# Optimization experiments

Hardware: AMD Instinct MI355X
Metric: run time of the kernel (lower is better)

## Reference

```python
import jax, jax.numpy as jnp
import numpy as np

N = 50000   # nodes
C = 128     # num_channels
E = 800000  # edges (before self loops)
P = 8192    # pos/neg pairs
L = 2       # num_layers
NEG_SLOPE = 0.2  # GATv2Conv default negative_slope


def setup_inputs() -> dict:
    key = jax.random.key(0)
    ks = jax.random.split(key, 10)
    x = jax.random.normal(ks[0], (N, C), dtype=jnp.float32)
    edge_index = jax.random.randint(ks[1], (2, E), 0, N)
    true_pairs = jax.random.randint(ks[2], (P, 2), 0, N)
    false_pairs = jax.random.randint(ks[3], (P, 2), 0, N)
    s = 1.0 / np.sqrt(C)
    # GATv2Conv params per layer (heads=1, share_weights=False): lin_l, lin_r, att, bias
    Wl = jax.random.normal(ks[4], (L, C, C), dtype=jnp.float32) * s
    Wr = jax.random.normal(ks[5], (L, C, C), dtype=jnp.float32) * s
    att_w = jax.random.normal(ks[6], (L, C), dtype=jnp.float32) * s
    bias = jnp.zeros((L, C), dtype=jnp.float32)
    # ConcatAndLogisticScorer classifier: Linear(2C,C) -> ReLU -> Linear(C,1) -> Sigmoid
    W1 = jax.random.normal(ks[7], (2 * C, C), dtype=jnp.float32) * (1.0 / np.sqrt(2 * C))
    b1 = jnp.zeros((C,), dtype=jnp.float32)
    W2 = jax.random.normal(ks[8], (C, 1), dtype=jnp.float32) * s
    b2 = jnp.zeros((1,), dtype=jnp.float32)
    return dict(x=x, edge_index=edge_index, true_pairs=true_pairs, false_pairs=false_pairs,
                Wl=Wl, Wr=Wr, att_w=att_w, bias=bias, W1=W1, b1=b1, W2=W2, b2=b2)


def _gatv2_layer(h, src, dst, Wl, Wr, a, b):
    # single-head GATv2: e_ij = a^T LeakyReLU(Wl h_j + Wr h_i); softmax over incoming edges of i
    n = h.shape[0]
    xl = h @ Wl  # [N,C] (source transform, also the message value)
    xr = h @ Wr  # [N,C] (target transform)
    z = xl[src] + xr[dst]                       # [E,C]
    z = jnp.where(z >= 0, z, NEG_SLOPE * z)     # leaky_relu
    e = z @ a                                   # [E]
    emax = jax.ops.segment_max(e, dst, num_segments=n)
    p = jnp.exp(e - emax[dst])
    denom = jax.ops.segment_sum(p, dst, num_segments=n)
    alpha = p / denom[dst]                      # edge softmax per dst node
    out = jax.ops.segment_sum(alpha[:, None] * xl[src], dst, num_segments=n)
    return out + b


def _gnn_and_score(x, src, dst, Wl, Wr, att_w, bias, W1, b1, W2, b2, true_pairs, false_pairs):
    h = x
    n_layers = Wl.shape[0]
    for l in range(n_layers):
        h = _gatv2_layer(h, src, dst, Wl[l], Wr[l], att_w[l], bias[l])
        if l < n_layers - 1:  # BasicGNN: activation between layers, not after last
            h = jax.nn.relu(h)
    pos = jnp.concatenate([h[true_pairs[:, 0]], h[true_pairs[:, 1]]], axis=-1)   # [P,2C]
    neg = jnp.concatenate([h[false_pairs[:, 0]], h[false_pairs[:, 1]]], axis=-1)  # [P,2C]
    v = jnp.concatenate([pos, neg], axis=0)  # [2P,2C]
    hid = jax.nn.relu(v @ W1 + b1)
    probs = jax.nn.sigmoid(hid @ W2 + b2)    # [2P,1]
    return pos, neg, probs


def reference(x, edge_index, true_pairs, false_pairs, Wl, Wr, att_w, bias, W1, b1, W2, b2):
    n = x.shape[0]
    loop = jnp.arange(n)  # GATv2Conv add_self_loops=True
    src = jnp.concatenate([edge_index[0], loop])
    dst = jnp.concatenate([edge_index[1], loop])
    pos, neg, probs = _gnn_and_score(x, src, dst, Wl, Wr, att_w, bias, W1, b1, W2, b2,
                                     true_pairs, false_pairs)
    npos = pos.shape[0]
    labels = jnp.concatenate([jnp.ones((npos, 1), jnp.float32),
                              jnp.zeros((probs.shape[0] - npos, 1), jnp.float32)], axis=0)
    pcl = jnp.clip(probs, 1e-7, 1.0 - 1e-7)  # BCELoss log clamping
    loss = -jnp.mean(labels * jnp.log(pcl) + (1.0 - labels) * jnp.log1p(-pcl))
    return pos, neg, probs, loss
```

## Files before the change

kernel.cpp:

```cpp
#include <hip/hip_runtime.h>
#include <math.h>

#define C 128
#define OVF_CAP 32768

typedef unsigned short ushort_t;
typedef short short8 __attribute__((ext_vector_type(8)));
typedef float floatx4 __attribute__((ext_vector_type(4)));
typedef float fx2 __attribute__((ext_vector_type(2)));

__device__ __forceinline__ ushort_t f2bf(float x) {
  unsigned u = __float_as_uint(x);
  unsigned r = (u + 0x7FFFu + ((u >> 16) & 1u)) >> 16;
  return (ushort_t)r;
}
__device__ __forceinline__ fx2 bf2f2(unsigned u) {
  fx2 r;
  r.x = __uint_as_float(u << 16);
  r.y = __uint_as_float(u & 0xFFFF0000u);
  return r;
}


__global__ void k_init_prep(int* __restrict__ deg, int* __restrict__ mark,
                            float* __restrict__ lossacc,
                            unsigned* __restrict__ done_cnt, int* __restrict__ ncnt,
                            int* __restrict__ ovf_cnt, int n,
                            const float* __restrict__ Wl, const float* __restrict__ Wr,
                            const float* __restrict__ W1,
                            ushort_t* __restrict__ wcat, ushort_t* __restrict__ w1t) {
  int idx = blockIdx.x * blockDim.x + threadIdx.x;
  if (idx < n) { deg[idx] = 0; mark[idx] = 0; }
  if (idx == 0) { lossacc[0] = 0.f; done_cnt[0] = 0u; ncnt[0] = 0; ovf_cnt[0] = 0; }
  const int NCAT = 2 * 256 * 128;
  if (idx < NCAT) {
    int l = idx >> 15;
    int rem = idx & 32767;
    int nn = rem >> 7;
    int k = rem & 127;
    float v = (nn < 128) ? Wl[l * C * C + k * C + nn] : Wr[l * C * C + k * C + (nn - 128)];
    wcat[idx] = f2bf(v);
  } else if (idx < NCAT + 128 * 256) {
    int j = idx - NCAT;
    int nn = j >> 8;
    int k = j & 255;
    w1t[j] = f2bf(W1[k * C + nn]);
  }
}


__global__ void k_conv_hist(const float* __restrict__ x, ushort_t* __restrict__ xb, int total4,
                            const int* __restrict__ ei, int* __restrict__ deg,
                            int* __restrict__ col32, int* __restrict__ ovf,
                            int* __restrict__ ovf_cnt, int E, int ET,
                            const int* __restrict__ tp, const int* __restrict__ fp, int npair2,
                            int* __restrict__ mark, int* __restrict__ nlist, int* __restrict__ ncnt) {
  int i = blockIdx.x * blockDim.x + threadIdx.x;
  if (i < total4) {
    float4 v = ((const float4*)x)[i];
    ushort4 s;
    s.x = f2bf(v.x); s.y = f2bf(v.y); s.z = f2bf(v.z); s.w = f2bf(v.w);
    ((ushort4*)xb)[i] = s;
  }
  if (i < ET) {
    int s, d;
    if (i < E) { s = ei[i]; d = ei[E + i]; }
    else { s = i - E; d = i - E; }
    int p = atomicAdd(&deg[d], 1);
    if (p < 32) {
      col32[(d << 5) + p] = s;
    } else {
      int k = atomicAdd(ovf_cnt, 1);
      if (k < OVF_CAP) { ovf[2 * k] = d; ovf[2 * k + 1] = s; }
    }
  }
  if (i < 2 * npair2) {
    int node = (i < npair2) ? tp[i] : fp[i - npair2];
    if (atomicExch(&mark[node], 1) == 0) {
      int k = atomicAdd(ncnt, 1);
      nlist[k] = node;
    }
  }
}


__device__ __forceinline__ void gemm_body(
    const ushort_t* __restrict__ A, const ushort_t* __restrict__ Bt,
    int M, int K,
    ushort_t* __restrict__ outb0, ushort_t* __restrict__ outb1,
    int bx, int by) {
  int tid = threadIdx.x;
  int wave = tid >> 6, lane = tid & 63;
  int wm = (wave >> 1) * 64, wn = (wave & 1) * 64;
  int m_base = bx * 128 + wm;
  int lrow = lane & 15, lkg = lane >> 4;

  floatx4 acc[4][4];
  #pragma unroll
  for (int mi = 0; mi < 4; mi++)
    #pragma unroll
    for (int ni = 0; ni < 4; ni++)
      acc[mi][ni] = (floatx4){0.f, 0.f, 0.f, 0.f};

  const int ksteps = K >> 5;
  for (int ks = 0; ks < ksteps; ks++) {
    int koff = ks * 32 + lkg * 8;
    short8 af[4], bfr[4];
    #pragma unroll
    for (int mi = 0; mi < 4; mi++) {
      int gm = m_base + mi * 16 + lrow;
      gm = (gm < M) ? gm : (M - 1);
      af[mi] = *(const short8*)&A[(size_t)gm * K + koff];
    }
    #pragma unroll
    for (int ni = 0; ni < 4; ni++) {
      int gn = by * 128 + wn + ni * 16 + lrow;
      bfr[ni] = *(const short8*)&Bt[(size_t)gn * K + koff];
    }
    #pragma unroll
    for (int mi = 0; mi < 4; mi++)
      #pragma unroll
      for (int ni = 0; ni < 4; ni++)
        acc[mi][ni] = __builtin_amdgcn_mfma_f32_16x16x32_bf16(af[mi], bfr[ni], acc[mi][ni], 0, 0, 0);
  }

  ushort_t* outb = (by == 0) ? outb0 : outb1;
  #pragma unroll
  for (int mi = 0; mi < 4; mi++) {
    #pragma unroll
    for (int r = 0; r < 4; r++) {
      int gm = m_base + mi * 16 + lkg * 4 + r;
      if (gm >= M) continue;
      #pragma unroll
      for (int ni = 0; ni < 4; ni++) {
        int nl = wn + ni * 16 + lrow;
        outb[(size_t)gm * 128 + nl] = f2bf(acc[mi][ni][r]);
      }
    }
  }
}

__global__ __launch_bounds__(256) void gemm_mfma(
    const ushort_t* __restrict__ A, const ushort_t* __restrict__ Bt,
    int M, int K,
    ushort_t* __restrict__ outb0, ushort_t* __restrict__ outb1) {
  gemm_body(A, Bt, M, K, outb0, outb1, blockIdx.x, blockIdx.y);
}


__global__ __launch_bounds__(256) void gat_aggregate(
    const ushort_t* __restrict__ xl, const ushort_t* __restrict__ xr,
    const int* __restrict__ deg, const int* __restrict__ col32,
    const int* __restrict__ ovf, const int* __restrict__ ovf_cnt,
    const float* __restrict__ att, const float* __restrict__ bias,
    float* __restrict__ houtf, ushort_t* __restrict__ houtb,
    const int* __restrict__ nlist, const int* __restrict__ ncnt,
    int n, int do_relu) {
  int gwid = (int)((blockIdx.x * (size_t)blockDim.x + threadIdx.x) >> 6);
  int lane = threadIdx.x & 63;
  int wid;
  if (nlist) {
    if (gwid >= ncnt[0]) return;
    wid = nlist[gwid];
  } else {
    if (gwid >= n) return;
    wid = gwid;
  }
  int g = lane >> 4, p = lane & 15;
  int c0 = p * 8;
  const size_t i = wid;

  fx2 xri[4], av[4];
  {
    uint4 ur = *(const uint4*)&xr[i * C + c0];
    xri[0] = bf2f2(ur.x); xri[1] = bf2f2(ur.y);
    xri[2] = bf2f2(ur.z); xri[3] = bf2f2(ur.w);
    float4 a0 = *(const float4*)&att[c0];
    float4 a1 = *(const float4*)&att[c0 + 4];
    const float L2E = 1.44269504088896f;
    av[0] = (fx2){a0.x * L2E, a0.y * L2E}; av[1] = (fx2){a0.z * L2E, a0.w * L2E};
    av[2] = (fx2){a1.x * L2E, a1.y * L2E}; av[3] = (fx2){a1.z * L2E, a1.w * L2E};
  }

  int degc = deg[wid];
  int beg = wid << 5;
  int dmain = (degc < 32) ? degc : 32;
  int end = beg + dmain;
  float denom = 0.f;
  fx2 acc[4];
  #pragma unroll
  for (int q = 0; q < 4; q++) acc[q] = (fx2){0.f, 0.f};

  for (int base = beg; base < end; base += 8) {
    int e0 = base + g;
    int e1 = e0 + 4;
    unsigned j0 = min((unsigned)col32[e0], (unsigned)(n - 1));
    unsigned j1 = min((unsigned)col32[e1], (unsigned)(n - 1));
    uint4 r0 = *(const uint4*)&xl[((size_t)j0 << 7) + c0];
    uint4 r1 = *(const uint4*)&xl[((size_t)j1 << 7) + c0];
    fx2 x0[4], x1[4];
    x0[0] = bf2f2(r0.x); x0[1] = bf2f2(r0.y); x0[2] = bf2f2(r0.z); x0[3] = bf2f2(r0.w);
    x1[0] = bf2f2(r1.x); x1[1] = bf2f2(r1.y); x1[2] = bf2f2(r1.z); x1[3] = bf2f2(r1.w);

    fx2 d0 = (fx2){0.f, 0.f}, d1 = (fx2){0.f, 0.f};
    #pragma unroll
    for (int q = 0; q < 4; q++) {
      fx2 z0 = x0[q] + xri[q];
      fx2 z1 = x1[q] + xri[q];
      z0 = __builtin_elementwise_max(z0, z0 * 0.2f);
      z1 = __builtin_elementwise_max(z1, z1 * 0.2f);
      d0 = __builtin_elementwise_fma(z0, av[q], d0);
      d1 = __builtin_elementwise_fma(z1, av[q], d1);
    }
    float p0 = d0.x + d0.y;
    float p1 = d1.x + d1.y;
    #pragma unroll
    for (int off = 1; off <= 8; off <<= 1) {
      p0 += __shfl_xor(p0, off);
      p1 += __shfl_xor(p1, off);
    }
    float pe0 = (e0 < end) ? __builtin_amdgcn_exp2f(p0) : 0.f;
    float pe1 = (e1 < end) ? __builtin_amdgcn_exp2f(p1) : 0.f;
    denom += pe0 + pe1;
    fx2 v0 = (fx2){pe0, pe0}, v1 = (fx2){pe1, pe1};
    #pragma unroll
    for (int q = 0; q < 4; q++) {
      acc[q] = __builtin_elementwise_fma(v0, x0[q], acc[q]);
      acc[q] = __builtin_elementwise_fma(v1, x1[q], acc[q]);
    }
  }

  if (degc > 32) {
    int oc = ovf_cnt[0];
    oc = (oc < OVF_CAP) ? oc : OVF_CAP;
    for (int t = 0; t < oc; t++) {
      if (ovf[2 * t] != wid) continue;
      unsigned j0 = min((unsigned)ovf[2 * t + 1], (unsigned)(n - 1));
      uint4 r0 = *(const uint4*)&xl[((size_t)j0 << 7) + c0];
      fx2 x0[4];
      x0[0] = bf2f2(r0.x); x0[1] = bf2f2(r0.y); x0[2] = bf2f2(r0.z); x0[3] = bf2f2(r0.w);
      fx2 d0 = (fx2){0.f, 0.f};
      #pragma unroll
      for (int q = 0; q < 4; q++) {
        fx2 z0 = x0[q] + xri[q];
        z0 = __builtin_elementwise_max(z0, z0 * 0.2f);
        d0 = __builtin_elementwise_fma(z0, av[q], d0);
      }
      float p0 = d0.x + d0.y;
      #pragma unroll
      for (int off = 1; off <= 8; off <<= 1)
        p0 += __shfl_xor(p0, off);
      float pe = (g == 0) ? __builtin_amdgcn_exp2f(p0) : 0.f;
      denom += pe;
      fx2 v0 = (fx2){pe, pe};
      #pragma unroll
      for (int q = 0; q < 4; q++)
        acc[q] = __builtin_elementwise_fma(v0, x0[q], acc[q]);
    }
  }

  #pragma unroll
  for (int off = 16; off <= 32; off <<= 1) {
    denom += __shfl_xor(denom, off);
    #pragma unroll
    for (int q = 0; q < 4; q++) {
      acc[q].x += __shfl_xor(acc[q].x, off);
      acc[q].y += __shfl_xor(acc[q].y, off);
    }
  }

  if (g == 0) {
    float inv = 1.f / denom;
    float4 b0 = *(const float4*)&bias[c0];
    float4 b1 = *(const float4*)&bias[c0 + 4];
    float o[8];
    o[0] = acc[0].x*inv + b0.x; o[1] = acc[0].y*inv + b0.y;
    o[2] = acc[1].x*inv + b0.z; o[3] = acc[1].y*inv + b0.w;
    o[4] = acc[2].x*inv + b1.x; o[5] = acc[2].y*inv + b1.y;
    o[6] = acc[3].x*inv + b1.z; o[7] = acc[3].y*inv + b1.w;
    if (do_relu) {
      #pragma unroll
      for (int c = 0; c < 8; c++) o[c] = fmaxf(o[c], 0.f);
    }
    if (houtf) {
      *(float4*)&houtf[i * C + c0]     = make_float4(o[0], o[1], o[2], o[3]);
      *(float4*)&houtf[i * C + c0 + 4] = make_float4(o[4], o[5], o[6], o[7]);
    } else {
      short8 s;
      #pragma unroll
      for (int c = 0; c < 8; c++) s[c] = (short)f2bf(o[c]);
      *(short8*)&houtb[i * C + c0] = s;
    }
  }
}


__global__ __launch_bounds__(256) void gemm_scorer(
    const float* __restrict__ h, const int* __restrict__ tp, const int* __restrict__ fp,
    const ushort_t* __restrict__ w1t, float* __restrict__ out_pos,
    const float* __restrict__ b1, const float* __restrict__ W2,
    const float* __restrict__ b2, float* __restrict__ probs_out,
    float* __restrict__ lossacc, unsigned* __restrict__ done_cnt,
    float* __restrict__ out_loss, int P2, int P) {
  __shared__ float lhalf[2][128];
  __shared__ float red[128];
  int tid = threadIdx.x;
  int wave = tid >> 6, lane = tid & 63;
  int wm = (wave >> 1) * 64, wn = (wave & 1) * 64;
  int m_base = blockIdx.x * 128 + wm;
  int lrow = lane & 15, lkg = lane >> 4;
  int half = P2 >> 1;
  bool emit = (wn == 0);

  int n0[4], n1[4];
  #pragma unroll
  for (int mi = 0; mi < 4; mi++) {
    int gm = m_base + mi * 16 + lrow;
    const int* pr = (gm < half) ? &tp[(size_t)gm * 2] : &fp[(size_t)(gm - half) * 2];
    n0[mi] = pr[0];
    n1[mi] = pr[1];
  }

  floatx4 acc[4][4];
  #pragma unroll
  for (int mi = 0; mi < 4; mi++)
    #pragma unroll
    for (int ni = 0; ni < 4; ni++)
      acc[mi][ni] = (floatx4){0.f, 0.f, 0.f, 0.f};

  #pragma unroll
  for (int ks = 0; ks < 8; ks++) {
    int koff = ks * 32 + lkg * 8;
    int chan = koff & 127;
    short8 af[4], bfr[4];
    #pragma unroll
    for (int mi = 0; mi < 4; mi++) {
      int node = (ks < 4) ? n0[mi] : n1[mi];
      const float* src = &h[(size_t)node * C + chan];
      float4 lo = *(const float4*)src;
      float4 hi = *(const float4*)(src + 4);
      if (emit) {
        int gm = m_base + mi * 16 + lrow;
        *(float4*)&out_pos[(size_t)gm * 256 + koff]     = lo;
        *(float4*)&out_pos[(size_t)gm * 256 + koff + 4] = hi;
      }
      short8 a;
      a[0] = (short)f2bf(lo.x); a[1] = (short)f2bf(lo.y);
      a[2] = (short)f2bf(lo.z); a[3] = (short)f2bf(lo.w);
      a[4] = (short)f2bf(hi.x); a[5] = (short)f2bf(hi.y);
      a[6] = (short)f2bf(hi.z); a[7] = (short)f2bf(hi.w);
      af[mi] = a;
    }
    #pragma unroll
    for (int ni = 0; ni < 4; ni++) {
      int gn = wn + ni * 16 + lrow;
      bfr[ni] = *(const short8*)&w1t[(size_t)gn * 256 + koff];
    }
    #pragma unroll
    for (int mi = 0; mi < 4; mi++)
      #pragma unroll
      for (int ni = 0; ni < 4; ni++)
        acc[mi][ni] = __builtin_amdgcn_mfma_f32_16x16x32_bf16(af[mi], bfr[ni], acc[mi][ni], 0, 0, 0);
  }

  float b1v[4], w2v[4];
  #pragma unroll
  for (int ni = 0; ni < 4; ni++) {
    int nl = wn + ni * 16 + lrow;
    b1v[ni] = b1[nl];
    w2v[ni] = W2[nl];
  }
  #pragma unroll
  for (int mi = 0; mi < 4; mi++) {
    #pragma unroll
    for (int r = 0; r < 4; r++) {
      float ps = 0.f;
      #pragma unroll
      for (int ni = 0; ni < 4; ni++) {
        float v = fmaxf(acc[mi][ni][r] + b1v[ni], 0.f);
        ps = fmaf(v, w2v[ni], ps);
      }
      #pragma unroll
      for (int off = 1; off <= 8; off <<= 1)
        ps += __shfl_xor(ps, off);
      if (lrow == 0)
        lhalf[wn ? 1 : 0][wm + mi * 16 + lkg * 4 + r] = ps;
    }
  }
  __syncthreads();

  float term = 0.f;
  if (tid < 128) {
    int gr = blockIdx.x * 128 + tid;
    float s = lhalf[0][tid] + lhalf[1][tid] + b2[0];
    float pv = 1.f / (1.f + expf(-s));
    probs_out[gr] = pv;
    float pcl = fminf(fmaxf(pv, 1e-7f), 1.f - 1e-7f);
    term = (gr < P) ? logf(pcl) : log1pf(-pcl);
    red[tid] = term;
  }
  __syncthreads();
  if (tid < 64) red[tid] += red[tid + 64];
  __syncthreads();
  if (tid < 32) red[tid] += red[tid + 32];
  __syncthreads();
  if (tid == 0) {
    float s = 0.f;
    #pragma unroll
    for (int k = 0; k < 32; k++) s += red[k];
    atomicAdd(lossacc, s);
    __threadfence();
    unsigned prev = atomicAdd(done_cnt, 1u);
    if (prev == gridDim.x - 1) {
      float total = atomicAdd(lossacc, 0.f);
      out_loss[0] = -total / (float)P2;
    }
  }
}


extern "C" void kernel_launch(void* const* d_in, const int* in_sizes, int n_in,
                              void* d_out, int out_size, void* d_ws, size_t ws_size,
                              hipStream_t stream) {
  const float* x    = (const float*)d_in[0];
  const int*   ei   = (const int*)d_in[1];
  const int*   tp   = (const int*)d_in[2];
  const int*   fp   = (const int*)d_in[3];
  const float* Wl   = (const float*)d_in[4];
  const float* Wr   = (const float*)d_in[5];
  const float* att  = (const float*)d_in[6];
  const float* bias = (const float*)d_in[7];
  const float* W1   = (const float*)d_in[8];
  const float* b1   = (const float*)d_in[9];
  const float* W2   = (const float*)d_in[10];
  const float* b2   = (const float*)d_in[11];

  int N  = in_sizes[0] / C;
  int E  = in_sizes[1] / 2;
  int P  = in_sizes[2] / 2;
  int ET = E + N;
  int P2 = 2 * P;
  int npair2 = 2 * P;

  float* out       = (float*)d_out;
  float* out_pos   = out;
  float* out_probs = out + (size_t)P2 * 2 * C;
  float* out_loss  = out_probs + P2;

  char* w = (char*)d_ws;
  size_t NCb2 = (size_t)N * C * 2;
  ushort_t* x_bf  = (ushort_t*)w;  w += NCb2;
  ushort_t* xl_bf = (ushort_t*)w;  w += NCb2;
  ushort_t* xr_bf = (ushort_t*)w;  w += NCb2;
  ushort_t* h1_bf = (ushort_t*)w;  w += NCb2;
  float* h1f = (float*)w;          w += (size_t)N * C * 4;
  ushort_t* wcat = (ushort_t*)w;   w += (size_t)2 * 256 * 128 * 2;
  ushort_t* w1t  = (ushort_t*)w;   w += (size_t)128 * 256 * 2;
  int* deg     = (int*)w;  w += (size_t)N * 4;
  int* mark    = (int*)w;  w += (size_t)N * 4;
  int* nlist   = (int*)w;  w += (size_t)(2 * npair2) * 4;
  int* col32   = (int*)w;  w += (size_t)N * 32 * 4;
  int* ovf     = (int*)w;  w += (size_t)OVF_CAP * 2 * 4;
  float* lossacc = (float*)w;  w += 16;
  unsigned* done_cnt = (unsigned*)w;  w += 16;
  int* ncnt    = (int*)w;  w += 16;
  int* ovf_cnt = (int*)w;

  const int tB = 256;
  int total4 = N * C / 4;

  k_init_prep<<<384, tB, 0, stream>>>(deg, mark, lossacc, done_cnt, ncnt, ovf_cnt, N,
                                      Wl, Wr, W1, wcat, w1t);
  k_conv_hist<<<(total4 + tB - 1) / tB, tB, 0, stream>>>(
      x, x_bf, total4, ei, deg, col32, ovf, ovf_cnt, E, ET,
      tp, fp, npair2, mark, nlist, ncnt);

  int gblk = (N + 127) / 128;

  gemm_mfma<<<dim3(gblk, 2), tB, 0, stream>>>(x_bf, wcat, N, C, xl_bf, xr_bf);
  gat_aggregate<<<(N * 64 + tB - 1) / tB, tB, 0, stream>>>(
      xl_bf, xr_bf, deg, col32, ovf, ovf_cnt, att, bias, nullptr, h1_bf,
      nullptr, nullptr, N, 1);

  gemm_mfma<<<dim3(gblk, 2), tB, 0, stream>>>(h1_bf, wcat + (size_t)256 * 128, N, C, xl_bf, xr_bf);
  int lblk = (2 * npair2 * 64 + tB - 1) / tB;
  gat_aggregate<<<lblk, tB, 0, stream>>>(
      xl_bf, xr_bf, deg, col32, ovf, ovf_cnt, att + C, bias + C, h1f, nullptr,
      nlist, ncnt, N, 0);

  gemm_scorer<<<P2 / 128, tB, 0, stream>>>(
      h1f, tp, fp, w1t, out_pos, b1, W2, b2, out_probs,
      lossacc, done_cnt, out_loss, P2, P);
}
```

Before: 200.0 us.

## Split edge bucketing into count pass and scatter fused with first GEMM

The histogram kernel now only records each edge's atomic slot position into a new per-edge array. The scatter into the col32 buckets and overflow list moves into extra blocks of the first GEMM launch, so it runs alongside the MFMA work. The aim is to shorten the histogram kernel's critical path by overlapping the scattered writes with GEMM. The cost is an extra ET-sized position array written and then read back, plus a second read of edge indices.

Result: faster. 193.3 us, median of 2 (-3.4%).

```diff
diff --git a/kernel.cpp b/kernel.cpp
--- a/kernel.cpp
+++ b/kernel.cpp
@@ -51,8 +51,7 @@
 
 __global__ void k_conv_hist(const float* __restrict__ x, ushort_t* __restrict__ xb, int total4,
                             const int* __restrict__ ei, int* __restrict__ deg,
-                            int* __restrict__ col32, int* __restrict__ ovf,
-                            int* __restrict__ ovf_cnt, int E, int ET,
+                            int* __restrict__ pos, int E, int ET,
                             const int* __restrict__ tp, const int* __restrict__ fp, int npair2,
                             int* __restrict__ mark, int* __restrict__ nlist, int* __restrict__ ncnt) {
   int i = blockIdx.x * blockDim.x + threadIdx.x;
@@ -63,16 +62,8 @@
     ((ushort4*)xb)[i] = s;
   }
   if (i < ET) {
-    int s, d;
-    if (i < E) { s = ei[i]; d = ei[E + i]; }
-    else { s = i - E; d = i - E; }
-    int p = atomicAdd(&deg[d], 1);
-    if (p < 32) {
-      col32[(d << 5) + p] = s;
-    } else {
-      int k = atomicAdd(ovf_cnt, 1);
-      if (k < OVF_CAP) { ovf[2 * k] = d; ovf[2 * k + 1] = s; }
-    }
+    int d = (i < E) ? ei[E + i] : (i - E);
+    pos[i] = atomicAdd(&deg[d], 1);
   }
   if (i < 2 * npair2) {
     int node = (i < npair2) ? tp[i] : fp[i - npair2];
@@ -145,6 +136,35 @@
     int M, int K,
     ushort_t* __restrict__ outb0, ushort_t* __restrict__ outb1) {
   gemm_body(A, Bt, M, K, outb0, outb1, blockIdx.x, blockIdx.y);
+}
+
+
+__global__ __launch_bounds__(256) void k_gemm_scatter(
+    const ushort_t* __restrict__ A, const ushort_t* __restrict__ Bt,
+    int M, int K,
+    ushort_t* __restrict__ outb0, ushort_t* __restrict__ outb1, int gb,
+    const int* __restrict__ ei, const int* __restrict__ pos,
+    int* __restrict__ col32, int* __restrict__ ovf, int* __restrict__ ovf_cnt,
+    int E, int ET) {
+  int bx = blockIdx.x;
+  if (bx < gb) {
+    gemm_body(A, Bt, M, K, outb0, outb1, bx, blockIdx.y);
+  } else {
+    int chunk = (bx - gb) * 2 + blockIdx.y;
+    int e = chunk * 256 + threadIdx.x;
+    if (e < ET) {
+      int s, d;
+      if (e < E) { s = ei[e]; d = ei[E + e]; }
+      else { s = e - E; d = e - E; }
+      int p = pos[e];
+      if (p < 32) {
+        col32[(d << 5) + p] = s;
+      } else {
+        int k = atomicAdd(ovf_cnt, 1);
+        if (k < OVF_CAP) { ovf[2 * k] = d; ovf[2 * k + 1] = s; }
+      }
+    }
+  }
 }
 
 
@@ -459,6 +479,7 @@
   int* deg     = (int*)w;  w += (size_t)N * 4;
   int* mark    = (int*)w;  w += (size_t)N * 4;
   int* nlist   = (int*)w;  w += (size_t)(2 * npair2) * 4;
+  int* pos     = (int*)w;  w += (size_t)ET * 4;
   int* col32   = (int*)w;  w += (size_t)N * 32 * 4;
   int* ovf     = (int*)w;  w += (size_t)OVF_CAP * 2 * 4;
   float* lossacc = (float*)w;  w += 16;
@@ -472,12 +493,15 @@
   k_init_prep<<<384, tB, 0, stream>>>(deg, mark, lossacc, done_cnt, ncnt, ovf_cnt, N,
                                       Wl, Wr, W1, wcat, w1t);
   k_conv_hist<<<(total4 + tB - 1) / tB, tB, 0, stream>>>(
-      x, x_bf, total4, ei, deg, col32, ovf, ovf_cnt, E, ET,
-      tp, fp, npair2, mark, nlist, ncnt);
+      x, x_bf, total4, ei, deg, pos, E, ET, tp, fp, npair2, mark, nlist, ncnt);
 
   int gblk = (N + 127) / 128;
-
-  gemm_mfma<<<dim3(gblk, 2), tB, 0, stream>>>(x_bf, wcat, N, C, xl_bf, xr_bf);
+  int schunks = (ET + tB - 1) / tB;
+  int sxtra = (schunks + 1) / 2;
+
+  k_gemm_scatter<<<dim3(gblk + sxtra, 2), tB, 0, stream>>>(
+      x_bf, wcat, N, C, xl_bf, xr_bf, gblk, ei, pos, col32, ovf, ovf_cnt, E, ET);
+
   gat_aggregate<<<(N * 64 + tB - 1) / tB, tB, 0, stream>>>(
       xl_bf, xr_bf, deg, col32, ovf, ovf_cnt, att, bias, nullptr, h1_bf,
       nullptr, nullptr, N, 1);
```
